# Kernel tuning notes

Measured on AMD Instinct MI355X. Metric: run time of the kernel, lower is better.

## Reference

```python
import jax, jax.numpy as jnp
import numpy as np

N, L, LEADS = 512, 640, 3
COND_DIM, NUM_K, DIM_K = 1, 100, 5
FLAT = 256 * 79  # 20224, from conv stack trace


def _leaky(x):
    return jnp.where(x >= 0, x, 0.2 * x)


def _sn(w, u):
    # PyTorch spectral_norm: one power iteration (u, v detached), sigma = u^T W v
    wm = w.reshape(w.shape[0], -1)
    v = wm.T @ u
    v = v / (jnp.linalg.norm(v) + 1e-12)
    u2 = wm @ v
    u2 = u2 / (jnp.linalg.norm(u2) + 1e-12)
    u2 = jax.lax.stop_gradient(u2)
    v = jax.lax.stop_gradient(v)
    sigma = u2 @ (wm @ v)
    return w / sigma


def _conv1d(x, w, b, stride, pad):
    y = jax.lax.conv_general_dilated(
        x, w, window_strides=(stride,), padding=[(pad, pad)],
        dimension_numbers=('NCH', 'OIH', 'NCH'))
    return y + b[None, :, None]


def setup_inputs() -> dict:
    key = jax.random.key(0)
    ks = jax.random.split(key, 16)
    g = lambda k, shp, s: (jax.random.normal(k, shp, dtype=jnp.float32) * s)
    inp = {
        'ecg': jax.random.normal(ks[0], (N, L, LEADS), dtype=jnp.float32),
        'condition': jax.random.randint(ks[1], (N, 1), 0, 4),
        'w1': g(ks[2], (64, LEADS, 5), 0.2), 'b1': jnp.zeros((64,), jnp.float32),
        'u1': jax.random.normal(ks[3], (64,), dtype=jnp.float32),
        'w2': g(ks[4], (128, 64, 7), 0.05), 'b2': jnp.zeros((128,), jnp.float32),
        'u2': jax.random.normal(ks[5], (128,), dtype=jnp.float32),
        'w3': g(ks[6], (256, 128, 9), 0.03), 'b3': jnp.zeros((256,), jnp.float32),
        'u3': jax.random.normal(ks[7], (256,), dtype=jnp.float32),
        'emb': g(ks[8], (4, COND_DIM), 1.0),
        'cond_w': g(ks[9], (50, COND_DIM), 0.5), 'cond_b': jnp.zeros((50,), jnp.float32),
        'mb_w': g(ks[10], (FLAT, NUM_K * DIM_K), 0.01),
        'fc_w': g(ks[11], (1, FLAT + NUM_K + 50), 0.01), 'fc_b': jnp.zeros((1,), jnp.float32),
    }
    return inp


def reference(ecg, condition, w1, b1, u1, w2, b2, u2, w3, b3, u3,
              emb, cond_w, cond_b, mb_w, fc_w, fc_b):
    # condition embedding -> Linear(cond_dim, 50)
    cemb = emb[condition[:, 0]]                       # [N, cond_dim]
    cond = cemb @ cond_w.T + cond_b                   # [N, 50]

    x = ecg.transpose(0, 2, 1)                        # [N, 3, 640]
    x = _leaky(_conv1d(x, _sn(w1, u1), b1, 2, 4))     # [N, 64, 322]
    x = _leaky(_conv1d(x, _sn(w2, u2), b2, 2, 3))     # [N, 128, 161]
    x = _leaky(_conv1d(x, _sn(w3, u3), b3, 2, 2))     # [N, 256, 79]
    flat = x.reshape(x.shape[0], -1)                  # [N, 20224]

    # minibatch discrimination
    act = (flat @ mb_w).reshape(-1, NUM_K, DIM_K)     # [N, K, D]
    l1 = jnp.abs(act[:, None] - act[None, :]).sum(-1)  # [N, N, K]
    feats = jnp.exp(-l1).sum(axis=1)                  # [N, K]

    out = jnp.concatenate([flat, feats, cond], axis=1)
    return out @ fc_w.T + fc_b                        # [N, 1]
```

## Files before the change

### kernel.cpp

```cpp
#include <hip/hip_runtime.h>
#include <math.h>

#define NB 512
#define LIN 640
#define NLEADS 3
#define L1O 322
#define L2O 161
#define L3O 79
#define C1N 64
#define C2N 128
#define C3N 256
#define FLATSZ 20224
#define NUMK 100
#define DIMK 5
#define SPLITK 16

typedef __attribute__((ext_vector_type(8))) short short8;
typedef __attribute__((ext_vector_type(4))) float f32x4;

__device__ __forceinline__ unsigned short f2bf(float x){
  unsigned u = __builtin_bit_cast(unsigned, x);
  unsigned r = u + 0x7FFFu + ((u >> 16) & 1u);
  return (unsigned short)(r >> 16);
}
__device__ __forceinline__ float bf2f(unsigned short x){
  unsigned u = ((unsigned)x) << 16;
  return __builtin_bit_cast(float, u);
}

__device__ __forceinline__ float block_reduce_sum(float val, float* red){
#pragma unroll
  for(int off=32; off>0; off>>=1) val += __shfl_down(val, off, 64);
  int lane = threadIdx.x & 63;
  int wv = threadIdx.x >> 6;
  if(lane==0) red[wv] = val;
  __syncthreads();
  int nw = blockDim.x >> 6;
  float r = red[0];
  for(int i=1;i<nw;i++) r += red[i];
  __syncthreads();
  return r;
}

__global__ __launch_bounds__(256)
void sn_pass1(const float* __restrict__ w1, const float* __restrict__ u1,
              const float* __restrict__ w2, const float* __restrict__ u2,
              const float* __restrict__ w3, const float* __restrict__ u3,
              float* __restrict__ v_all, float* __restrict__ ss){
  __shared__ float red[4];
  int b = blockIdx.x, tid = threadIdx.x;
  const float* w; const float* u; int O, C, off, c, widx;
  if(b==0){ w=w1; u=u1; O=64;  C=15;   off=0;   c=tid;            widx=0; }
  else if(b<3){ w=w2; u=u2; O=128; C=448; off=16;  c=(b-1)*256+tid; widx=1; }
  else { w=w3; u=u3; O=256; C=1152; off=464; c=(b-3)*256+tid;      widx=2; }
  float vv = 0.f;
  if(c < C){
    for(int o=0;o<O;o+=4){
      vv += w[(o+0)*C+c]*u[o+0] + w[(o+1)*C+c]*u[o+1]
          + w[(o+2)*C+c]*u[o+2] + w[(o+3)*C+c]*u[o+3];
    }
    v_all[off + c] = vv;
  }
  float ps = (c < C) ? vv*vv : 0.f;
  float tot = block_reduce_sum(ps, red);
  if(tid==0) atomicAdd(&ss[widx], tot);
}

__global__ __launch_bounds__(256)
void sn_pass2(const float* __restrict__ w1, const float* __restrict__ w2,
              const float* __restrict__ w3, const float* __restrict__ v_all,
              float* __restrict__ Sun){
  int b = blockIdx.x, tid = threadIdx.x;
  int lane = tid & 63, wv = tid >> 6;
  const float* w; int C, off, o, widx;
  if(b < 16){ w=w1; C=15;   off=0;   o=b*4+wv;      widx=0; }
  else if(b < 48){ w=w2; C=448; off=16;  o=(b-16)*4+wv; widx=1; }
  else { w=w3; C=1152; off=464; o=(b-48)*4+wv;          widx=2; }
  float t = 0.f;
  for(int c=lane; c<C; c+=64) t += w[o*C+c]*v_all[off+c];
#pragma unroll
  for(int s=32; s>0; s>>=1) t += __shfl_down(t, s, 64);
  if(lane==0) atomicAdd(&Sun[widx], t*t);
}

__global__ void sn_final(const float* __restrict__ ss, const float* __restrict__ Sun,
                         float* __restrict__ scale){
  int tid = threadIdx.x;
  if(tid < 3){
    float inv = 1.f/(sqrtf(ss[tid])+1e-12f);
    float S = Sun[tid]*inv*inv;
    scale[tid] = (sqrtf(S)+1e-12f)/S;
  }
}

__global__ void wprep_kernel(const float* __restrict__ w1, const float* __restrict__ w2,
                             const float* __restrict__ w3, const float* __restrict__ scale,
                             unsigned short* __restrict__ w1p, unsigned short* __restrict__ w2p,
                             unsigned short* __restrict__ w3p){
  int idx = blockIdx.x*256 + threadIdx.x;
  float s1 = scale[0], s2 = scale[1], s3 = scale[2];
  if(idx < C1N*32){
    int o = idx >> 5, kk = idx & 31;
    w1p[idx] = (kk < 15) ? f2bf(w1[o*15+kk]*s1) : 0;
  }
  if(idx < C2N*448){
    int o = idx / 448, k2 = idx - o*448;
    int r = k2 >> 6, i = k2 & 63;
    w2p[idx] = f2bf(w2[o*448 + i*7 + r]*s2);
  }
  if(idx < C3N*1152){
    int o = idx / 1152, k2 = idx - o*1152;
    int r = k2 >> 7, i = k2 & 127;
    w3p[idx] = f2bf(w3[o*1152 + i*9 + r]*s3);
  }
}

__global__ __launch_bounds__(256, 4)
void conv12_mfma(const float* __restrict__ ecg, const unsigned short* __restrict__ w1p,
                 const float* __restrict__ b1, const unsigned short* __restrict__ w2p,
                 const float* __restrict__ b2, unsigned short* __restrict__ y2t){
  __shared__ unsigned short slabs[13600];
  __shared__ unsigned short B1s[6656];
  int n = blockIdx.x, tile = blockIdx.y, tid = threadIdx.x;
  int lane = tid & 63, w = tid >> 6;
  int c0    = tile ? 189 : 0;
  int tbase = tile ? 96  : 0;
  int suboff= tile ? -94 : 2;

  {
    uint4 z = {0u,0u,0u,0u};
    uint4* zd = (uint4*)slabs;
#pragma unroll
    for(int q=0;q<7;q++){
      int f = q*256 + tid;
      if(f < 1700) zd[f] = z;
    }
  }
  const float* eb = ecg + (size_t)n*LIN*NLEADS;
#pragma unroll
  for(int q=0;q<26;q++){
    int e = q*256 + tid;
    int tp = e >> 5, kk = e & 31;
    unsigned short v = 0;
    if(kk < 15){
      int i = kk/5, r = kk - i*5;
      int p = 2*(c0 + tp) - 4 + r;
      if((unsigned)p < (unsigned)LIN) v = f2bf(eb[p*NLEADS + i]);
    }
    B1s[tp*32 + kk] = v;
  }
  __syncthreads();

  {
    short8 a1 = *(const short8*)(w1p + ((w*16 + (lane&15))<<5) + (lane>>4)*8);
    f32x4 zero = {0.f,0.f,0.f,0.f};
#pragma unroll
    for(int half=0; half<2; half++){
      int nt0 = half*7, ntc = half ? 6 : 7;
      f32x4 c1[7];
      for(int j=0;j<ntc;j++){
        short8 b = *(const short8*)(B1s + (((nt0+j)*16 + (lane&15))<<5) + (lane>>4)*8);
        c1[j] = __builtin_amdgcn_mfma_f32_16x16x32_bf16(a1, b, zero, 0, 0, 0);
      }
#pragma unroll
      for(int reg=0;reg<4;reg++){
        int o = w*16 + (lane>>4)*4 + reg;
        float bias = b1[o];
        for(int j=0;j<ntc;j++){
          int tp = (nt0+j)*16 + (lane&15);
          int t1 = c0 + tp;
          int sub = (t1>>1) + suboff;
          if(t1 < L1O && sub < 100){
            float v = c1[j][reg] + bias;
            v = v>=0.f ? v : 0.2f*v;
            slabs[((t1&1)?6800:0) + sub*68 + o] = f2bf(v);
          }
        }
      }
    }
  }
  __syncthreads();

  f32x4 zero = {0.f,0.f,0.f,0.f};
  f32x4 acc[2][6];
#pragma unroll
  for(int i=0;i<2;i++)
#pragma unroll
    for(int j=0;j<6;j++) acc[i][j] = zero;

  const unsigned short* w2base = w2p + ((size_t)(w*2*16 + (lane&15)))*448 + (lane>>4)*8;
  short8 a_cur[2];
  a_cur[0] = *(const short8*)(w2base);
  a_cur[1] = *(const short8*)(w2base + 16*448);

  for(int ck=0; ck<14; ck++){
    short8 a_nxt[2];
    if(ck < 13){
      a_nxt[0] = *(const short8*)(w2base + (ck+1)*32);
      a_nxt[1] = *(const short8*)(w2base + 16*448 + (ck+1)*32);
    }
    int r = ck >> 1, i0 = (ck & 1)*32;
    int p = (r+1) & 1;
    int m = ((r-3) - p) >> 1;
    int base = (p?6800:0) + (m+2 + (lane&15))*68 + i0 + (lane>>4)*8;
    short8 b[6];
#pragma unroll
    for(int nt=0;nt<6;nt++)
      b[nt] = *(const short8*)(slabs + base + nt*16*68);
#pragma unroll
    for(int mm=0;mm<2;mm++)
#pragma unroll
      for(int nt=0;nt<6;nt++)
        acc[mm][nt] = __builtin_amdgcn_mfma_f32_16x16x32_bf16(a_cur[mm], b[nt], acc[mm][nt], 0, 0, 0);
    if(ck < 13){ a_cur[0] = a_nxt[0]; a_cur[1] = a_nxt[1]; }
  }

  __syncthreads();
  unsigned short* trans = slabs;
#pragma unroll
  for(int mm=0;mm<2;mm++){
#pragma unroll
    for(int reg=0;reg<4;reg++){
      int o = (w*2+mm)*16 + (lane>>4)*4 + reg;
      float bias = b2[o];
#pragma unroll
      for(int nt=0;nt<6;nt++){
        int tl = nt*16 + (lane&15);
        int t = tbase + tl;
        if(t < L2O){
          float v = acc[mm][nt][reg] + bias;
          v = v>=0.f ? v : 0.2f*v;
          trans[tl*136 + o] = f2bf(v);
        }
      }
    }
  }
  __syncthreads();
  {
    int rows = tile ? 65 : 96;
    uint4* dstg = (uint4*)(y2t + (size_t)n*20608 + tbase*128);
#pragma unroll
    for(int q=0;q<6;q++){
      int f = q*256 + tid;
      int row = f >> 4, c8 = f & 15;
      if(row < rows)
        dstg[row*16 + c8] = *(const uint4*)(trans + row*136 + c8*8);
    }
  }
}

__global__ __launch_bounds__(256, 2)
void conv3_mfma(const unsigned short* __restrict__ y2t, const unsigned short* __restrict__ w3p,
                const float* __restrict__ b3, unsigned short* __restrict__ flatbf){
  __shared__ unsigned short lds[22712];
  int n = blockIdx.x, tid = threadIdx.x;
  int lane = tid & 63, w = tid >> 6;

  if(tid < 136){
    lds[tid] = 0;
    lds[82*136 + tid] = 0;
    lds[83*136 + tid] = 0;
    lds[11424 + tid] = 0;
    lds[11424 + 81*136 + tid] = 0;
    lds[11424 + 82*136 + tid] = 0;
  }
  {
    const uint4* src = (const uint4*)(y2t + (size_t)n*20608);
#pragma unroll
    for(int q=0;q<11;q++){
      int f = q*256 + tid;
      if(f < 2576){
        int g = f >> 4, c8 = f & 15;
        int sub = g >> 1, p = g & 1;
        *(uint4*)(lds + (p ? 11424 : 0) + (sub+1)*136 + c8*8) = src[(size_t)g*16 + c8];
      }
    }
  }

  f32x4 zero = {0.f,0.f,0.f,0.f};
  f32x4 acc[4][5];
#pragma unroll
  for(int i=0;i<4;i++)
#pragma unroll
    for(int j=0;j<5;j++) acc[i][j] = zero;

  const unsigned short* wbase = w3p + ((size_t)(w*64) + (lane&15))*1152 + (lane>>4)*8;
  short8 abuf[3][4];
#pragma unroll
  for(int d=0; d<2; d++)
#pragma unroll
    for(int mm=0;mm<4;mm++)
      abuf[d][mm] = *(const short8*)(wbase + mm*16*1152 + d*32);
  __syncthreads();

#pragma unroll
  for(int ck=0; ck<36; ck++){
    const int cur = ck % 3;
    const int nxt = (ck+2) % 3;
    if(ck+2 < 36){
      int kc = (ck+2)*32;
#pragma unroll
      for(int mm=0;mm<4;mm++)
        abuf[nxt][mm] = *(const short8*)(wbase + mm*16*1152 + kc);
    }
    int r = ck >> 2, i0 = (ck & 3) * 32;
    int cbase = ((r & 1) ? 11424 : 0) + (r >> 1)*136 + i0 + (lane>>4)*8;
    short8 b[5];
#pragma unroll
    for(int nt=0;nt<5;nt++){
      int t = nt*16 + (lane&15);
      b[nt] = *(const short8*)(lds + cbase + t*136);
    }
#pragma unroll
    for(int mm=0;mm<4;mm++)
#pragma unroll
      for(int nt=0;nt<5;nt++)
        acc[mm][nt] = __builtin_amdgcn_mfma_f32_16x16x32_bf16(abuf[cur][mm], b[nt], acc[mm][nt], 0, 0, 0);
  }
#pragma unroll
  for(int mm=0;mm<4;mm++){
#pragma unroll
    for(int reg=0;reg<4;reg++){
      int o = w*64 + mm*16 + (lane>>4)*4 + reg;
      float bias = b3[o];
#pragma unroll
      for(int nt=0;nt<5;nt++){
        int t = nt*16 + (lane&15);
        if(t < L3O){
          float v = acc[mm][nt][reg] + bias;
          v = v>=0.f ? v : 0.2f*v;
          flatbf[(size_t)n*FLATSZ + o*L3O + t] = f2bf(v);
        }
      }
    }
  }
}

__global__ __launch_bounds__(256)
void mbw_transpose(const float* __restrict__ mbw, unsigned short* __restrict__ mbwT){
  __shared__ unsigned short tile[32][36];
  int k0 = blockIdx.x*32, n0 = blockIdx.y*32, tid = threadIdx.x;
  int r = tid >> 3, c4 = (tid & 7) * 4;
  int nbase = n0 + c4;
  if(nbase + 3 < 500){
    float4 v = *(const float4*)(mbw + (size_t)(k0+r)*500 + nbase);
    tile[r][c4+0] = f2bf(v.x);
    tile[r][c4+1] = f2bf(v.y);
    tile[r][c4+2] = f2bf(v.z);
    tile[r][c4+3] = f2bf(v.w);
  } else {
#pragma unroll
    for(int j=0;j<4;j++){
      int nn = nbase + j;
      float v = (nn < 500) ? mbw[(size_t)(k0+r)*500 + nn] : 0.f;
      tile[r][c4+j] = f2bf(v);
    }
  }
  __syncthreads();
  int nl = tid >> 3, kq = (tid & 7) * 4;
  unsigned short t0 = tile[kq+0][nl], t1 = tile[kq+1][nl];
  unsigned short t2 = tile[kq+2][nl], t3 = tile[kq+3][nl];
  uint2 p;
  p.x = (unsigned)t0 | ((unsigned)t1 << 16);
  p.y = (unsigned)t2 | ((unsigned)t3 << 16);
  *(uint2*)(mbwT + (size_t)(n0+nl)*FLATSZ + k0 + kq) = p;
}

__global__ __launch_bounds__(256)
void mb_gemm_mfma(const unsigned short* __restrict__ flatbf, const unsigned short* __restrict__ mbwT,
                  float* __restrict__ part){
  __shared__ unsigned short As[64*32];
  __shared__ unsigned short Bs[64*32];
  int tid = threadIdx.x;
  int lane = tid & 63, w = tid >> 6;
  int m0 = blockIdx.x*64, n0 = blockIdx.y*64, bz = blockIdx.z;
  int t_start = bz*39 + (bz<8 ? bz : 8);
  int t_count = 39 + (bz<8 ? 1 : 0);
  int k0 = t_start*32;
  f32x4 zero = {0.f,0.f,0.f,0.f};
  f32x4 acc[4];
#pragma unroll
  for(int i=0;i<4;i++) acc[i] = zero;
  int arow = tid >> 2, acol = (tid & 3) * 8;
  for(int t=0; t<t_count; t++, k0+=32){
    __syncthreads();
    ((uint4*)As)[tid] = *(const uint4*)(flatbf + (size_t)(m0+arow)*FLATSZ + k0 + acol);
    ((uint4*)Bs)[tid] = *(const uint4*)(mbwT  + (size_t)(n0+arow)*FLATSZ + k0 + acol);
    __syncthreads();
    short8 a = *(const short8*)(As + (w*16 + (lane&15))*32 + (lane>>4)*8);
#pragma unroll
    for(int nt=0;nt<4;nt++){
      short8 b = *(const short8*)(Bs + (nt*16 + (lane&15))*32 + (lane>>4)*8);
      acc[nt] = __builtin_amdgcn_mfma_f32_16x16x32_bf16(a, b, acc[nt], 0, 0, 0);
    }
  }
  float* po = part + (size_t)bz*NB*500;
#pragma unroll
  for(int nt=0;nt<4;nt++){
#pragma unroll
    for(int reg=0;reg<4;reg++){
      int m = m0 + w*16 + (lane>>4)*4 + reg;
      int c = n0 + nt*16 + (lane&15);
      if(c < 500) po[(size_t)m*500 + c] = acc[nt][reg];
    }
  }
}

__global__ void mb_reduce_kernel(const float* __restrict__ part, float* __restrict__ actT){
  int idx = blockIdx.x*256 + threadIdx.x;
  float s = 0.f;
#pragma unroll
  for(int z=0;z<SPLITK;z++) s += part[(size_t)z*NB*500 + idx];
  int n = idx/500, c = idx - n*500;
  actT[(size_t)c*NB + n] = s;
}

__global__ __launch_bounds__(256)
void feats_kernel(const float* __restrict__ actT, float* __restrict__ feats){
  __shared__ float ash[4][50];
  __shared__ float pred[4][4];
  int i0 = blockIdx.x*4, k0 = blockIdx.y*10;
  int tid = threadIdx.x, lane = tid & 63, wv = tid >> 6;
  if(tid < 200){
    int ii = tid/50, c = tid - ii*50;
    ash[ii][c] = actT[(size_t)(k0*5+c)*NB + i0 + ii];
  }
  __syncthreads();
  const float LOG2E = 1.4426950408889634f;
  int j1 = tid, j2 = tid + 256;
  for(int kk=0; kk<10; kk++){
    const float* r0 = actT + (size_t)(k0+kk)*5*NB;
    float xa0=r0[j1], xa1=r0[NB+j1], xa2=r0[2*NB+j1], xa3=r0[3*NB+j1], xa4=r0[4*NB+j1];
    float xb0=r0[j2], xb1=r0[NB+j2], xb2=r0[2*NB+j2], xb3=r0[3*NB+j2], xb4=r0[4*NB+j2];
    float f[4];
#pragma unroll
    for(int ii=0; ii<4; ii++){
      float a0=ash[ii][kk*5+0], a1=ash[ii][kk*5+1], a2=ash[ii][kk*5+2],
            a3=ash[ii][kk*5+3], a4=ash[ii][kk*5+4];
      float la = fabsf(xa0-a0)+fabsf(xa1-a1)+fabsf(xa2-a2)+fabsf(xa3-a3)+fabsf(xa4-a4);
      float lb = fabsf(xb0-a0)+fabsf(xb1-a1)+fabsf(xb2-a2)+fabsf(xb3-a3)+fabsf(xb4-a4);
      f[ii] = exp2f(-LOG2E*la) + exp2f(-LOG2E*lb);
    }
#pragma unroll
    for(int ii=0; ii<4; ii++){
      float v = f[ii];
#pragma unroll
      for(int s=32; s>0; s>>=1) v += __shfl_down(v, s, 64);
      if(lane==0) pred[wv][ii] = v;
    }
    __syncthreads();
    if(tid < 4){
      float v = pred[0][tid] + pred[1][tid] + pred[2][tid] + pred[3][tid];
      feats[(size_t)(i0+tid)*NUMK + k0 + kk] = v;
    }
    __syncthreads();
  }
}

__global__ void final_kernel(const unsigned short* __restrict__ flatbf, const float* __restrict__ feats,
                             const int* __restrict__ condition, const float* __restrict__ emb,
                             const float* __restrict__ cond_w, const float* __restrict__ cond_b,
                             const float* __restrict__ fc_w, const float* __restrict__ fc_b,
                             float* __restrict__ out){
  __shared__ float red[4];
  int n = blockIdx.x, tid = threadIdx.x;
  float s = 0.f;
  const unsigned short* fr = flatbf + (size_t)n*FLATSZ;
  for(int q=tid; q<FLATSZ/8; q+=256){
    uint4 u = *(const uint4*)(fr + q*8);
    float4 wa = *(const float4*)(fc_w + q*8);
    float4 wb = *(const float4*)(fc_w + q*8 + 4);
    s += bf2f((unsigned short)(u.x & 0xffff))*wa.x + bf2f((unsigned short)(u.x >> 16))*wa.y
       + bf2f((unsigned short)(u.y & 0xffff))*wa.z + bf2f((unsigned short)(u.y >> 16))*wa.w
       + bf2f((unsigned short)(u.z & 0xffff))*wb.x + bf2f((unsigned short)(u.z >> 16))*wb.y
       + bf2f((unsigned short)(u.w & 0xffff))*wb.z + bf2f((unsigned short)(u.w >> 16))*wb.w;
  }
  for(int k=tid;k<NUMK;k+=256) s += feats[n*NUMK+k]*fc_w[FLATSZ+k];
  float ce = emb[condition[n]];
  for(int j=tid;j<50;j+=256) s += (ce*cond_w[j]+cond_b[j])*fc_w[FLATSZ+NUMK+j];
  s = block_reduce_sum(s, red);
  if(tid==0) out[n] = s + fc_b[0];
}

extern "C" void kernel_launch(void* const* d_in, const int* in_sizes, int n_in,
                              void* d_out, int out_size, void* d_ws, size_t ws_size,
                              hipStream_t stream) {
  const float* ecg   = (const float*)d_in[0];
  const int*   cond  = (const int*)  d_in[1];
  const float* w1    = (const float*)d_in[2];
  const float* b1    = (const float*)d_in[3];
  const float* u1    = (const float*)d_in[4];
  const float* w2    = (const float*)d_in[5];
  const float* b2    = (const float*)d_in[6];
  const float* u2    = (const float*)d_in[7];
  const float* w3    = (const float*)d_in[8];
  const float* b3    = (const float*)d_in[9];
  const float* u3    = (const float*)d_in[10];
  const float* emb   = (const float*)d_in[11];
  const float* condw = (const float*)d_in[12];
  const float* condb = (const float*)d_in[13];
  const float* mbw   = (const float*)d_in[14];
  const float* fcw   = (const float*)d_in[15];
  const float* fcb   = (const float*)d_in[16];

  float* ws = (float*)d_ws;
  float* scale = ws;
  float* ssbuf = ws + 16;
  float* Sunbuf= ws + 24;
  float* v_all = ws + 32;
  unsigned short* w1p  = (unsigned short*)(ws + 1648);
  unsigned short* w2p  = (unsigned short*)(ws + 2672);
  unsigned short* w3p  = (unsigned short*)(ws + 31344);
  unsigned short* y2t  = (unsigned short*)(ws + 178800);
  unsigned short* mbwT = (unsigned short*)(ws + 178800);
  float* part  = ws + 5454448;
  float* actT  = ws + 9550448;
  float* feats = ws + 9806448;
  unsigned short* flatbf = (unsigned short*)(ws + 9857648);

  hipMemsetAsync((char*)d_ws + 64, 0, 64, stream);
  sn_pass1<<<8, 256, 0, stream>>>(w1,u1,w2,u2,w3,u3, v_all, ssbuf);
  sn_pass2<<<112, 256, 0, stream>>>(w1,w2,w3, v_all, Sunbuf);
  sn_final<<<1, 64, 0, stream>>>(ssbuf, Sunbuf, scale);
  wprep_kernel<<<1152, 256, 0, stream>>>(w1, w2, w3, scale, w1p, w2p, w3p);
  conv12_mfma<<<dim3(NB,2), 256, 0, stream>>>(ecg, w1p, b1, w2p, b2, y2t);
  conv3_mfma<<<NB, 256, 0, stream>>>(y2t, w3p, b3, flatbf);
  mbw_transpose<<<dim3(632,16), 256, 0, stream>>>(mbw, mbwT);
  mb_gemm_mfma<<<dim3(8,8,SPLITK), 256, 0, stream>>>(flatbf, mbwT, part);
  mb_reduce_kernel<<<1000, 256, 0, stream>>>(part, actT);
  feats_kernel<<<dim3(128,10), 256, 0, stream>>>(actT, feats);
  final_kernel<<<NB, 256, 0, stream>>>(flatbf, feats, cond, emb, condw, condb, fcw, fcb, (float*)d_out);
}
```

Before: 314.2 us.

## Fuse conv1/conv2 with conv3 into one per-sample kernel keeping y2 in LDS

Merges the conv12 and conv3 kernels into a single kernel with one block per sample. The block loops over both conv2 tiles and writes layer-2 activations straight into an LDS buffer laid out the way conv3 reads it. This removes the global round trip of the y2 intermediate and one kernel launch. In exchange, grid parallelism for conv1/2 is halved (512 blocks instead of 1024), LDS use per block grows, and the conv1 input staging is split into halves to fit. Occupancy drops to the two-blocks-per-CU bound.

```diff
diff --git a/kernel.cpp b/kernel.cpp
--- a/kernel.cpp
+++ b/kernel.cpp
@@ -115,52 +115,71 @@
   }
 }
 
-__global__ __launch_bounds__(256, 4)
-void conv12_mfma(const float* __restrict__ ecg, const unsigned short* __restrict__ w1p,
-                 const float* __restrict__ b1, const unsigned short* __restrict__ w2p,
-                 const float* __restrict__ b2, unsigned short* __restrict__ y2t){
+__global__ __launch_bounds__(256, 2)
+void conv123_mfma(const float* __restrict__ ecg, const unsigned short* __restrict__ w1p,
+                  const float* __restrict__ b1, const unsigned short* __restrict__ w2p,
+                  const float* __restrict__ b2, const unsigned short* __restrict__ w3p,
+                  const float* __restrict__ b3, unsigned short* __restrict__ flatbf){
+  __shared__ unsigned short y2buf[22712];
   __shared__ unsigned short slabs[13600];
-  __shared__ unsigned short B1s[6656];
-  int n = blockIdx.x, tile = blockIdx.y, tid = threadIdx.x;
+  __shared__ unsigned short B1s[3584];
+  int n = blockIdx.x, tid = threadIdx.x;
   int lane = tid & 63, w = tid >> 6;
-  int c0    = tile ? 189 : 0;
-  int tbase = tile ? 96  : 0;
-  int suboff= tile ? -94 : 2;
-
-  {
-    uint4 z = {0u,0u,0u,0u};
-    uint4* zd = (uint4*)slabs;
-#pragma unroll
-    for(int q=0;q<7;q++){
-      int f = q*256 + tid;
-      if(f < 1700) zd[f] = z;
-    }
-  }
+
+  if(tid < 136){
+    y2buf[tid] = 0;
+    y2buf[82*136 + tid] = 0;
+    y2buf[83*136 + tid] = 0;
+    y2buf[11424 + tid] = 0;
+    y2buf[11424 + 81*136 + tid] = 0;
+    y2buf[11424 + 82*136 + tid] = 0;
+  }
+
   const float* eb = ecg + (size_t)n*LIN*NLEADS;
-#pragma unroll
-  for(int q=0;q<26;q++){
-    int e = q*256 + tid;
-    int tp = e >> 5, kk = e & 31;
-    unsigned short v = 0;
-    if(kk < 15){
-      int i = kk/5, r = kk - i*5;
-      int p = 2*(c0 + tp) - 4 + r;
-      if((unsigned)p < (unsigned)LIN) v = f2bf(eb[p*NLEADS + i]);
-    }
-    B1s[tp*32 + kk] = v;
-  }
-  __syncthreads();
-
-  {
+  f32x4 zero4 = {0.f,0.f,0.f,0.f};
+
+  for(int tile=0; tile<2; tile++){
+    int c0    = tile ? 189 : 0;
+    int tbase = tile ? 96  : 0;
+    int suboff= tile ? -94 : 2;
+
+    __syncthreads();
+    {
+      uint4 z = {0u,0u,0u,0u};
+      uint4* zd = (uint4*)slabs;
+#pragma unroll
+      for(int q=0;q<7;q++){
+        int f = q*256 + tid;
+        if(f < 1700) zd[f] = z;
+      }
+    }
+
     short8 a1 = *(const short8*)(w1p + ((w*16 + (lane&15))<<5) + (lane>>4)*8);
-    f32x4 zero = {0.f,0.f,0.f,0.f};
 #pragma unroll
     for(int half=0; half<2; half++){
-      int nt0 = half*7, ntc = half ? 6 : 7;
+      const int tp0 = half*112;
+      const int nt0 = half*7;
+      const int ntc = half ? 6 : 7;
+      const int rows = half ? 96 : 112;
+      __syncthreads();
+      for(int q=0;q<14;q++){
+        int e = q*256 + tid;
+        if(e < rows*32){
+          int tpl = e >> 5, kk = e & 31;
+          unsigned short v = 0;
+          if(kk < 15){
+            int i = kk/5, r = kk - i*5;
+            int p = 2*(c0 + tp0 + tpl) - 4 + r;
+            if((unsigned)p < (unsigned)LIN) v = f2bf(eb[p*NLEADS + i]);
+          }
+          B1s[tpl*32 + kk] = v;
+        }
+      }
+      __syncthreads();
       f32x4 c1[7];
       for(int j=0;j<ntc;j++){
-        short8 b = *(const short8*)(B1s + (((nt0+j)*16 + (lane&15))<<5) + (lane>>4)*8);
-        c1[j] = __builtin_amdgcn_mfma_f32_16x16x32_bf16(a1, b, zero, 0, 0, 0);
+        short8 b = *(const short8*)(B1s + ((((nt0+j)*16 + (lane&15)) - tp0)<<5) + (lane>>4)*8);
+        c1[j] = __builtin_amdgcn_mfma_f32_16x16x32_bf16(a1, b, zero4, 0, 0, 0);
       }
 #pragma unroll
       for(int reg=0;reg<4;reg++){
@@ -178,111 +197,67 @@
         }
       }
     }
+    __syncthreads();
+
+    f32x4 acc[2][6];
+#pragma unroll
+    for(int i=0;i<2;i++)
+#pragma unroll
+      for(int j=0;j<6;j++) acc[i][j] = zero4;
+
+    const unsigned short* w2base = w2p + ((size_t)(w*2*16 + (lane&15)))*448 + (lane>>4)*8;
+    short8 a_cur[2];
+    a_cur[0] = *(const short8*)(w2base);
+    a_cur[1] = *(const short8*)(w2base + 16*448);
+
+    for(int ck=0; ck<14; ck++){
+      short8 a_nxt[2];
+      if(ck < 13){
+        a_nxt[0] = *(const short8*)(w2base + (ck+1)*32);
+        a_nxt[1] = *(const short8*)(w2base + 16*448 + (ck+1)*32);
+      }
+      int r = ck >> 1, i0 = (ck & 1)*32;
+      int p = (r+1) & 1;
+      int m = ((r-3) - p) >> 1;
+      int base = (p?6800:0) + (m+2 + (lane&15))*68 + i0 + (lane>>4)*8;
+      short8 b[6];
+#pragma unroll
+      for(int nt=0;nt<6;nt++)
+        b[nt] = *(const short8*)(slabs + base + nt*16*68);
+#pragma unroll
+      for(int mm=0;mm<2;mm++)
+#pragma unroll
+        for(int nt=0;nt<6;nt++)
+          acc[mm][nt] = __builtin_amdgcn_mfma_f32_16x16x32_bf16(a_cur[mm], b[nt], acc[mm][nt], 0, 0, 0);
+      if(ck < 13){ a_cur[0] = a_nxt[0]; a_cur[1] = a_nxt[1]; }
+    }
+
+#pragma unroll
+    for(int mm=0;mm<2;mm++){
+#pragma unroll
+      for(int reg=0;reg<4;reg++){
+        int o = (w*2+mm)*16 + (lane>>4)*4 + reg;
+        float bias = b2[o];
+#pragma unroll
+        for(int nt=0;nt<6;nt++){
+          int tl = nt*16 + (lane&15);
+          int t = tbase + tl;
+          if(t < L2O){
+            float v = acc[mm][nt][reg] + bias;
+            v = v>=0.f ? v : 0.2f*v;
+            y2buf[((t&1)?11424:0) + ((t>>1)+1)*136 + o] = f2bf(v);
+          }
+        }
+      }
+    }
   }
   __syncthreads();
 
-  f32x4 zero = {0.f,0.f,0.f,0.f};
-  f32x4 acc[2][6];
-#pragma unroll
-  for(int i=0;i<2;i++)
-#pragma unroll
-    for(int j=0;j<6;j++) acc[i][j] = zero;
-
-  const unsigned short* w2base = w2p + ((size_t)(w*2*16 + (lane&15)))*448 + (lane>>4)*8;
-  short8 a_cur[2];
-  a_cur[0] = *(const short8*)(w2base);
-  a_cur[1] = *(const short8*)(w2base + 16*448);
-
-  for(int ck=0; ck<14; ck++){
-    short8 a_nxt[2];
-    if(ck < 13){
-      a_nxt[0] = *(const short8*)(w2base + (ck+1)*32);
-      a_nxt[1] = *(const short8*)(w2base + 16*448 + (ck+1)*32);
-    }
-    int r = ck >> 1, i0 = (ck & 1)*32;
-    int p = (r+1) & 1;
-    int m = ((r-3) - p) >> 1;
-    int base = (p?6800:0) + (m+2 + (lane&15))*68 + i0 + (lane>>4)*8;
-    short8 b[6];
-#pragma unroll
-    for(int nt=0;nt<6;nt++)
-      b[nt] = *(const short8*)(slabs + base + nt*16*68);
-#pragma unroll
-    for(int mm=0;mm<2;mm++)
-#pragma unroll
-      for(int nt=0;nt<6;nt++)
-        acc[mm][nt] = __builtin_amdgcn_mfma_f32_16x16x32_bf16(a_cur[mm], b[nt], acc[mm][nt], 0, 0, 0);
-    if(ck < 13){ a_cur[0] = a_nxt[0]; a_cur[1] = a_nxt[1]; }
-  }
-
-  __syncthreads();
-  unsigned short* trans = slabs;
-#pragma unroll
-  for(int mm=0;mm<2;mm++){
-#pragma unroll
-    for(int reg=0;reg<4;reg++){
-      int o = (w*2+mm)*16 + (lane>>4)*4 + reg;
-      float bias = b2[o];
-#pragma unroll
-      for(int nt=0;nt<6;nt++){
-        int tl = nt*16 + (lane&15);
-        int t = tbase + tl;
-        if(t < L2O){
-          float v = acc[mm][nt][reg] + bias;
-          v = v>=0.f ? v : 0.2f*v;
-          trans[tl*136 + o] = f2bf(v);
-        }
-      }
-    }
-  }
-  __syncthreads();
-  {
-    int rows = tile ? 65 : 96;
-    uint4* dstg = (uint4*)(y2t + (size_t)n*20608 + tbase*128);
-#pragma unroll
-    for(int q=0;q<6;q++){
-      int f = q*256 + tid;
-      int row = f >> 4, c8 = f & 15;
-      if(row < rows)
-        dstg[row*16 + c8] = *(const uint4*)(trans + row*136 + c8*8);
-    }
-  }
-}
-
-__global__ __launch_bounds__(256, 2)
-void conv3_mfma(const unsigned short* __restrict__ y2t, const unsigned short* __restrict__ w3p,
-                const float* __restrict__ b3, unsigned short* __restrict__ flatbf){
-  __shared__ unsigned short lds[22712];
-  int n = blockIdx.x, tid = threadIdx.x;
-  int lane = tid & 63, w = tid >> 6;
-
-  if(tid < 136){
-    lds[tid] = 0;
-    lds[82*136 + tid] = 0;
-    lds[83*136 + tid] = 0;
-    lds[11424 + tid] = 0;
-    lds[11424 + 81*136 + tid] = 0;
-    lds[11424 + 82*136 + tid] = 0;
-  }
-  {
-    const uint4* src = (const uint4*)(y2t + (size_t)n*20608);
-#pragma unroll
-    for(int q=0;q<11;q++){
-      int f = q*256 + tid;
-      if(f < 2576){
-        int g = f >> 4, c8 = f & 15;
-        int sub = g >> 1, p = g & 1;
-        *(uint4*)(lds + (p ? 11424 : 0) + (sub+1)*136 + c8*8) = src[(size_t)g*16 + c8];
-      }
-    }
-  }
-
-  f32x4 zero = {0.f,0.f,0.f,0.f};
-  f32x4 acc[4][5];
+  f32x4 acc3[4][5];
 #pragma unroll
   for(int i=0;i<4;i++)
 #pragma unroll
-    for(int j=0;j<5;j++) acc[i][j] = zero;
+    for(int j=0;j<5;j++) acc3[i][j] = zero4;
 
   const unsigned short* wbase = w3p + ((size_t)(w*64) + (lane&15))*1152 + (lane>>4)*8;
   short8 abuf[3][4];
@@ -291,7 +266,6 @@
 #pragma unroll
     for(int mm=0;mm<4;mm++)
       abuf[d][mm] = *(const short8*)(wbase + mm*16*1152 + d*32);
-  __syncthreads();
 
 #pragma unroll
   for(int ck=0; ck<36; ck++){
@@ -309,13 +283,13 @@
 #pragma unroll
     for(int nt=0;nt<5;nt++){
       int t = nt*16 + (lane&15);
-      b[nt] = *(const short8*)(lds + cbase + t*136);
+      b[nt] = *(const short8*)(y2buf + cbase + t*136);
     }
 #pragma unroll
     for(int mm=0;mm<4;mm++)
 #pragma unroll
       for(int nt=0;nt<5;nt++)
-        acc[mm][nt] = __builtin_amdgcn_mfma_f32_16x16x32_bf16(abuf[cur][mm], b[nt], acc[mm][nt], 0, 0, 0);
+        acc3[mm][nt] = __builtin_amdgcn_mfma_f32_16x16x32_bf16(abuf[cur][mm], b[nt], acc3[mm][nt], 0, 0, 0);
   }
 #pragma unroll
   for(int mm=0;mm<4;mm++){
@@ -327,7 +301,7 @@
       for(int nt=0;nt<5;nt++){
         int t = nt*16 + (lane&15);
         if(t < L3O){
-          float v = acc[mm][nt][reg] + bias;
+          float v = acc3[mm][nt][reg] + bias;
           v = v>=0.f ? v : 0.2f*v;
           flatbf[(size_t)n*FLATSZ + o*L3O + t] = f2bf(v);
         }
@@ -511,7 +485,6 @@
   unsigned short* w1p  = (unsigned short*)(ws + 1648);
   unsigned short* w2p  = (unsigned short*)(ws + 2672);
   unsigned short* w3p  = (unsigned short*)(ws + 31344);
-  unsigned short* y2t  = (unsigned short*)(ws + 178800);
   unsigned short* mbwT = (unsigned short*)(ws + 178800);
   float* part  = ws + 5454448;
   float* actT  = ws + 9550448;
@@ -523,8 +496,7 @@
   sn_pass2<<<112, 256, 0, stream>>>(w1,w2,w3, v_all, Sunbuf);
   sn_final<<<1, 64, 0, stream>>>(ssbuf, Sunbuf, scale);
   wprep_kernel<<<1152, 256, 0, stream>>>(w1, w2, w3, scale, w1p, w2p, w3p);
-  conv12_mfma<<<dim3(NB,2), 256, 0, stream>>>(ecg, w1p, b1, w2p, b2, y2t);
-  conv3_mfma<<<NB, 256, 0, stream>>>(y2t, w3p, b3, flatbf);
+  conv123_mfma<<<NB, 256, 0, stream>>>(ecg, w1p, b1, w2p, b2, w3p, b3, flatbf);
   mbw_transpose<<<dim3(632,16), 256, 0, stream>>>(mbw, mbwT);
   mb_gemm_mfma<<<dim3(8,8,SPLITK), 256, 0, stream>>>(flatbf, mbwT, part);
   mb_reduce_kernel<<<1000, 256, 0, stream>>>(part, actT);
```

After: 307.7 us. 1.02x faster.
